# Kernel tuning notes

Measured on AMD Instinct MI355X. Metric: run time of the kernel, lower is better.

Reference implementation:

```python
import jax, jax.numpy as jnp
import numpy as np

B, N, D, H, DK, DV = 2, 2048, 1024, 16, 64, 64
NEG = -1000000000.0
EPS = 1e-6


def setup_inputs() -> dict:
    key = jax.random.key(0)
    ks = jax.random.split(key, 8)
    s = 0.02
    return {
        "q": jax.random.normal(ks[0], (B, N, D), jnp.float32),
        "k": jax.random.normal(ks[1], (B, N, D), jnp.float32),
        "v": jax.random.normal(ks[2], (B, N, D), jnp.float32),
        "attn_mask": jnp.ones((B, N, N), jnp.int32),
        "Wq": jax.random.normal(ks[3], (D, H * DK), jnp.float32) * s,
        "Wk": jax.random.normal(ks[4], (D, H * DK), jnp.float32) * s,
        "Wv": jax.random.normal(ks[5], (D, H * DV), jnp.float32) * s,
        "Wo": jax.random.normal(ks[6], (H * DV, D), jnp.float32) * s,
        "gamma": jnp.ones((D,), jnp.float32),
        "beta": jnp.zeros((D,), jnp.float32),
    }


def reference(q, k, v, attn_mask, Wq, Wk, Wv, Wo, gamma, beta):
    b, n, _ = q.shape
    residual = q
    # project and split heads: (b, h, n, dk)
    qh = (q @ Wq).reshape(b, n, H, DK).transpose(0, 2, 1, 3)
    kh = (k @ Wk).reshape(b, n, H, DK).transpose(0, 2, 1, 3)
    vh = (v @ Wv).reshape(b, n, H, DV).transpose(0, 2, 1, 3)
    temperature = DK ** 0.5
    scores = jnp.einsum('bhnd,bhmd->bhnm', qh / temperature, kh)
    # external mask (masked where mask == 0), broadcast over heads
    scores = jnp.where(attn_mask[:, None, :, :] == 0, NEG, scores)
    # built-in causal mask (strictly upper triangle)
    causal = jnp.triu(jnp.ones((n, n), dtype=bool), k=1)
    scores = jnp.where(causal, NEG, scores)
    attn = jax.nn.softmax(scores, axis=-1)
    out = jnp.einsum('bhnm,bhmd->bnhd', attn, vh).reshape(b, n, H * DV)
    out = out @ Wo + residual
    # LayerNorm(eps=1e-6)
    mean = out.mean(-1, keepdims=True)
    var = ((out - mean) ** 2).mean(-1, keepdims=True)
    out = (out - mean) / jnp.sqrt(var + EPS) * gamma + beta
    return out, attn
```

## Files before the change

kernel.cpp:

```cpp
#include <hip/hip_runtime.h>
#include <hip/hip_bf16.h>
#include <stdint.h>

#define B_ 2
#define N_ 2048
#define D_ 1024
#define H_ 16
#define MM 4096
#define NN 1024
#define KK 1024

typedef __bf16 bf16;
typedef __bf16 bf16x8 __attribute__((ext_vector_type(8)));
typedef float f32x4 __attribute__((ext_vector_type(4)));

struct __align__(8) bf4 { bf16 v[4]; };

#define LDS_STRIDE 144

#define GLDS(gp, lp)                                                     \
    __builtin_amdgcn_global_load_lds(                                    \
        (const __attribute__((address_space(1))) void*)(gp),             \
        (__attribute__((address_space(3))) void*)(lp), 16, 0, 0)

__global__ __launch_bounds__(256) void k_cvt3(const float* __restrict__ q,
                                              const float* __restrict__ k,
                                              const float* __restrict__ v,
                                              bf16* __restrict__ qb,
                                              bf16* __restrict__ kb,
                                              bf16* __restrict__ vb) {
    const int z = blockIdx.y;
    const float* s = z == 0 ? q : z == 1 ? k : v;
    bf16* d = z == 0 ? qb : z == 1 ? kb : vb;
    size_t i = ((size_t)blockIdx.x * 256 + threadIdx.x) * 8;
    f32x4 a = *(const f32x4*)(s + i);
    f32x4 b = *(const f32x4*)(s + i + 4);
    bf16x8 o;
#pragma unroll
    for (int j = 0; j < 4; ++j) { o[j] = (bf16)a[j]; o[4 + j] = (bf16)b[j]; }
    *(bf16x8*)(d + i) = o;
}

__global__ void k_wtt(const float* __restrict__ W, bf16* __restrict__ Wt) {
    __shared__ float t[32][33];
    int bx = blockIdx.x * 32, by = blockIdx.y * 32;
    int tx = threadIdx.x, ty = threadIdx.y;
#pragma unroll
    for (int j = 0; j < 32; j += 8)
        t[ty + j][tx] = W[(size_t)(by + ty + j) * 1024 + bx + tx];
    __syncthreads();
#pragma unroll
    for (int j = 0; j < 32; j += 8)
        Wt[(size_t)(bx + ty + j) * 1024 + by + tx] = (bf16)t[tx][ty + j];
}

__global__ __launch_bounds__(256) void k_bits(const int* __restrict__ mask,
                                              uint32_t* __restrict__ bits) {
    size_t flat = (size_t)blockIdx.x * 256 + threadIdx.x;
    int col = (int)(flat & (N_ - 1));
    int row = (int)((flat >> 11) & (N_ - 1));
    bool ok = (mask[flat] != 0) && (col <= row);
    unsigned long long bal = __ballot(ok);
    if ((threadIdx.x & 63) == 0)
        *(unsigned long long*)(bits + (flat >> 5)) = bal;
}

__device__ __forceinline__ void mm_core(const bf16* __restrict__ A,
                                        const bf16* __restrict__ Bt,
                                        int bm0, int bn0,
                                        bf16* As, bf16* Bs,
                                        f32x4 (&acc)[4][4]) {
    const int tid = threadIdx.x, w = tid >> 6, lane = tid & 63;
    const int g = lane >> 4, li = lane & 15;
    const int wr = w >> 1, wc = w & 1;
    const int row = tid >> 3, cc = tid & 7;

    f32x4 zz = {0.f, 0.f, 0.f, 0.f};
#pragma unroll
    for (int mf = 0; mf < 4; ++mf)
#pragma unroll
        for (int nf = 0; nf < 4; ++nf) acc[mf][nf] = zz;

    auto stage = [&](int k0) {
#pragma unroll
        for (int c = 0; c < 4; ++c) {
            int ch = c * 256 + tid;
            int r = ch >> 3, cl = ch & 7;
            GLDS(A + (size_t)(bm0 + r) * KK + k0 + cl * 8,
                 As + ((size_t)c * 256 + w * 64) * 8);
        }
#pragma unroll
        for (int c = 0; c < 4; ++c) {
            int ch = c * 256 + tid;
            int r = ch >> 3, cl = ch & 7;
            GLDS(Bt + (size_t)(bn0 + r) * KK + k0 + cl * 8,
                 Bs + ((size_t)c * 256 + w * 64) * 8);
        }
    };
    (void)row; (void)cc;

    stage(0);
    for (int s = 0; s < KK / 64; ++s) {
        __syncthreads();
#pragma unroll
        for (int kk = 0; kk < 2; ++kk) {
            bf16x8 af[4], bfr[4];
#pragma unroll
            for (int i = 0; i < 4; ++i) {
                af[i] = *(const bf16x8*)(As + (wr * 64 + i * 16 + li) * 64 + kk * 32 + g * 8);
                bfr[i] = *(const bf16x8*)(Bs + (wc * 64 + i * 16 + li) * 64 + kk * 32 + g * 8);
            }
#pragma unroll
            for (int mf = 0; mf < 4; ++mf)
#pragma unroll
                for (int nf = 0; nf < 4; ++nf)
                    acc[mf][nf] = __builtin_amdgcn_mfma_f32_16x16x32_bf16(
                        af[mf], bfr[nf], acc[mf][nf], 0, 0, 0);
        }
        __syncthreads();
        if (s + 1 < KK / 64) stage((s + 1) * 64);
    }
}

__global__ __launch_bounds__(256) void k_proj(const bf16* __restrict__ qb,
                                              const bf16* __restrict__ kb,
                                              const bf16* __restrict__ vb,
                                              const bf16* __restrict__ WqT,
                                              const bf16* __restrict__ WkT,
                                              const bf16* __restrict__ WvT,
                                              bf16* __restrict__ Qh,
                                              bf16* __restrict__ Kh,
                                              bf16* __restrict__ Vt) {
    __shared__ __align__(16) bf16 As[128 * 64];
    __shared__ __align__(16) bf16 Bs[128 * 64];
    const int z = blockIdx.y;
    const bf16* A = z == 0 ? qb : z == 1 ? kb : vb;
    const bf16* Bt = z == 0 ? WqT : z == 1 ? WkT : WvT;
    int bid = blockIdx.x;
    int swz = (bid & 7) * 32 + (bid >> 3);
    int bm0 = (swz >> 3) * 128, bn0 = (swz & 7) * 128;

    f32x4 acc[4][4];
    mm_core(A, Bt, bm0, bn0, As, Bs, acc);

    const int tid = threadIdx.x, w = tid >> 6, lane = tid & 63;
    const int g = lane >> 4, li = lane & 15;
    const int wr = w >> 1, wc = w & 1;
    const float scale = (z == 0) ? 0.125f : 1.0f;

    if (z < 2) {
        bf16* C = (z == 0) ? Qh : Kh;
#pragma unroll
        for (int mf = 0; mf < 4; ++mf)
#pragma unroll
            for (int nf = 0; nf < 4; ++nf) {
                int m0 = bm0 + wr * 64 + mf * 16 + g * 4;
                int n = bn0 + wc * 64 + nf * 16 + li;
#pragma unroll
                for (int r = 0; r < 4; ++r)
                    C[(size_t)(m0 + r) * NN + n] = (bf16)(acc[mf][nf][r] * scale);
            }
    } else {
#pragma unroll
        for (int mf = 0; mf < 4; ++mf)
#pragma unroll
            for (int nf = 0; nf < 4; ++nf) {
                int m0 = bm0 + wr * 64 + mf * 16 + g * 4;
                int n = bn0 + wc * 64 + nf * 16 + li;
                int bq = m0 >> 11, tok = m0 & (N_ - 1);
                int hh = n >> 6, dv = n & 63;
                bf4 val;
#pragma unroll
                for (int r = 0; r < 4; ++r) val.v[r] = (bf16)acc[mf][nf][r];
                *(bf4*)(Vt + ((size_t)((bq * H_ + hh) * 64 + dv)) * N_ + tok) = val;
            }
    }
}

__global__ __launch_bounds__(256) void k_out(const bf16* __restrict__ Ob,
                                             const bf16* __restrict__ WoT,
                                             float* __restrict__ outp,
                                             const float* __restrict__ resid) {
    __shared__ __align__(16) bf16 As[128 * 64];
    __shared__ __align__(16) bf16 Bs[128 * 64];
    int bid = blockIdx.x;
    int swz = (bid & 7) * 32 + (bid >> 3);
    int bm0 = (swz >> 3) * 128, bn0 = (swz & 7) * 128;

    f32x4 acc[4][4];
    mm_core(Ob, WoT, bm0, bn0, As, Bs, acc);

    const int tid = threadIdx.x, w = tid >> 6, lane = tid & 63;
    const int g = lane >> 4, li = lane & 15;
    const int wr = w >> 1, wc = w & 1;
#pragma unroll
    for (int mf = 0; mf < 4; ++mf)
#pragma unroll
        for (int nf = 0; nf < 4; ++nf) {
            int m0 = bm0 + wr * 64 + mf * 16 + g * 4;
            int n = bn0 + wc * 64 + nf * 16 + li;
#pragma unroll
            for (int r = 0; r < 4; ++r) {
                size_t ix = (size_t)(m0 + r) * NN + n;
                outp[ix] = acc[mf][nf][r] + resid[ix];
            }
        }
}

__global__ __launch_bounds__(256) void k_attn(const bf16* __restrict__ Qh,
                                              const bf16* __restrict__ Kh,
                                              const bf16* __restrict__ Vt,
                                              const uint32_t* __restrict__ bits,
                                              float* __restrict__ attnp,
                                              bf16* __restrict__ Ob) {
    __shared__ __align__(16) char Qs[64 * LDS_STRIDE];
    __shared__ __align__(16) char Ks[2][64 * LDS_STRIDE];
    __shared__ __align__(16) char Vs[2][64 * LDS_STRIDE];
    __shared__ __align__(16) char Ps[64 * LDS_STRIDE];
    const int tid = threadIdx.x, lane = tid & 63, w = tid >> 6;
    const int g = lane >> 4, li = lane & 15;
    const int p = blockIdx.x, h = blockIdx.y, b = blockIdx.z;
    const int srow = tid >> 3, sc = tid & 7;
    const int myrow = w * 16 + li;

    const size_t kbase = ((size_t)b * N_) * D_ + h * 64;
    const size_t vbase = ((size_t)(b * H_ + h) * 64) * N_;
    f32x4 zz = {0.f, 0.f, 0.f, 0.f};

    bf16x8 ka, kb2, va, vb2;
    auto loadK = [&](int jt) {
        const char* ks = (const char*)Kh +
            (kbase + (size_t)(jt * 64 + srow) * D_ + sc * 8) * 2;
        ka = *(const bf16x8*)ks;
        kb2 = *(const bf16x8*)(ks + (size_t)32 * D_ * 2);
    };
    auto loadV = [&](int jt) {
        const char* vs = (const char*)Vt +
            (vbase + (size_t)srow * N_ + jt * 64 + sc * 8) * 2;
        va = *(const bf16x8*)vs;
        vb2 = *(const bf16x8*)(vs + (size_t)32 * N_ * 2);
    };
    auto writeK = [&](int bi) {
        *(bf16x8*)(Ks[bi] + srow * LDS_STRIDE + sc * 16) = ka;
        *(bf16x8*)(Ks[bi] + (srow + 32) * LDS_STRIDE + sc * 16) = kb2;
    };
    auto writeV = [&](int bi) {
        *(bf16x8*)(Vs[bi] + srow * LDS_STRIDE + sc * 16) = va;
        *(bf16x8*)(Vs[bi] + (srow + 32) * LDS_STRIDE + sc * 16) = vb2;
    };

    for (int half = 0; half < 2; ++half) {
        const int qt = half ? (31 - p) : p;
        const int i0 = qt << 6;
        const size_t abase = (((size_t)b * H_ + h) * N_ + i0) * (size_t)N_;

        __syncthreads();
        {
            const char* qsrc = (const char*)Qh +
                (kbase + (size_t)(i0 + srow) * D_ + sc * 8) * 2;
            bf16x8 t0 = *(const bf16x8*)qsrc;
            bf16x8 t1 = *(const bf16x8*)(qsrc + (size_t)32 * D_ * 2);
            *(bf16x8*)(Qs + srow * LDS_STRIDE + sc * 16) = t0;
            *(bf16x8*)(Qs + (srow + 32) * LDS_STRIDE + sc * 16) = t1;
        }
        const uint32_t* mrow = bits + (((size_t)b * N_ + i0 + myrow) << 6);

        float m = -1e30f, l = 0.f;
        loadK(0);
        writeK(0);
        for (int jt = 0; jt <= qt; ++jt) {
            if (jt < qt) loadK(jt + 1);
            uint2 mw = *(const uint2*)(mrow + (jt << 1));
            __syncthreads();
            const char* Kb = Ks[jt & 1];

            f32x4 s[4];
#pragma unroll
            for (int mf = 0; mf < 4; ++mf) s[mf] = zz;
#pragma unroll
            for (int kk = 0; kk < 2; ++kk) {
                const int kb = kk * 64 + (g << 4);
                bf16x8 qf = *(const bf16x8*)(Qs + myrow * LDS_STRIDE + kb);
#pragma unroll
                for (int mf = 0; mf < 4; ++mf) {
                    bf16x8 kf = *(const bf16x8*)(Kb + (mf * 16 + li) * LDS_STRIDE + kb);
                    s[mf] = __builtin_amdgcn_mfma_f32_16x16x32_bf16(kf, qf, s[mf], 0, 0, 0);
                }
            }
            if (jt < qt) writeK((jt + 1) & 1);

            float tmax = m;
#pragma unroll
            for (int mf = 0; mf < 4; ++mf) {
                uint32_t wsel = (mf < 2) ? mw.x : mw.y;
#pragma unroll
                for (int r = 0; r < 4; ++r) {
                    int sh = (mf & 1) * 16 + g * 4 + r;
                    float xv = ((wsel >> sh) & 1) ? s[mf][r] : -1e9f;
                    s[mf][r] = xv;
                    tmax = fmaxf(tmax, xv);
                }
            }
            tmax = fmaxf(tmax, __shfl_xor(tmax, 16));
            tmax = fmaxf(tmax, __shfl_xor(tmax, 32));
            float ps = 0.f;
#pragma unroll
            for (int mf = 0; mf < 4; ++mf)
#pragma unroll
                for (int r = 0; r < 4; ++r) ps += __expf(s[mf][r] - tmax);
            ps += __shfl_xor(ps, 16);
            ps += __shfl_xor(ps, 32);
            l = l * __expf(m - tmax) + ps;
            m = tmax;
        }
        const float linv = 1.0f / l;

        f32x4 oacc[4];
#pragma unroll
        for (int nf = 0; nf < 4; ++nf) oacc[nf] = zz;

        __syncthreads();
        loadK(0);
        loadV(0);
        writeK(0);
        writeV(0);
        for (int jt = 0; jt <= qt; ++jt) {
            if (jt < qt) { loadK(jt + 1); loadV(jt + 1); }
            uint2 mw = *(const uint2*)(mrow + (jt << 1));
            __syncthreads();
            const char* Kb = Ks[jt & 1];
            const char* Vb = Vs[jt & 1];

            f32x4 s[4];
#pragma unroll
            for (int mf = 0; mf < 4; ++mf) s[mf] = zz;
#pragma unroll
            for (int kk = 0; kk < 2; ++kk) {
                const int kb = kk * 64 + (g << 4);
                bf16x8 qf = *(const bf16x8*)(Qs + myrow * LDS_STRIDE + kb);
#pragma unroll
                for (int mf = 0; mf < 4; ++mf) {
                    bf16x8 kf = *(const bf16x8*)(Kb + (mf * 16 + li) * LDS_STRIDE + kb);
                    s[mf] = __builtin_amdgcn_mfma_f32_16x16x32_bf16(kf, qf, s[mf], 0, 0, 0);
                }
            }
            if (jt < qt) { writeK((jt + 1) & 1); writeV((jt + 1) & 1); }

#pragma unroll
            for (int mf = 0; mf < 4; ++mf) {
                uint32_t wsel = (mf < 2) ? mw.x : mw.y;
#pragma unroll
                for (int r = 0; r < 4; ++r) {
                    int sh = (mf & 1) * 16 + g * 4 + r;
                    float xv = ((wsel >> sh) & 1) ? s[mf][r] : -1e9f;
                    s[mf][r] = __expf(xv - m) * linv;
                }
                __builtin_nontemporal_store(s[mf],
                    (f32x4*)(attnp + abase + (size_t)myrow * N_ + (jt << 6) + mf * 16 + g * 4));
                bf4 pk;
#pragma unroll
                for (int r = 0; r < 4; ++r) pk.v[r] = (bf16)s[mf][r];
                *(bf4*)(Ps + myrow * LDS_STRIDE + (mf * 16 + g * 4) * 2) = pk;
            }
#pragma unroll
            for (int kk = 0; kk < 2; ++kk) {
                const int kb = kk * 64 + (g << 4);
                bf16x8 pf = *(const bf16x8*)(Ps + myrow * LDS_STRIDE + kb);
#pragma unroll
                for (int nf = 0; nf < 4; ++nf) {
                    bf16x8 vf = *(const bf16x8*)(Vb + (nf * 16 + li) * LDS_STRIDE + kb);
                    oacc[nf] = __builtin_amdgcn_mfma_f32_16x16x32_bf16(pf, vf, oacc[nf], 0, 0, 0);
                }
            }
        }
#pragma unroll
        for (int nf = 0; nf < 4; ++nf)
#pragma unroll
            for (int r = 0; r < 4; ++r) {
                int gi = i0 + w * 16 + g * 4 + r;
                Ob[((size_t)(b * N_ + gi)) * D_ + h * 64 + nf * 16 + li] = (bf16)oacc[nf][r];
            }
        int zc0 = i0 + 64;
        if (zc0 < N_) {
            int r = tid >> 2, tc = tid & 3;
            f32x4 z = zz;
            for (int c = zc0 + tc * 4; c < N_; c += 16)
                __builtin_nontemporal_store(z, (f32x4*)(attnp + abase + (size_t)r * N_ + c));
        }
    }
}

__global__ __launch_bounds__(256) void k_ln(float* __restrict__ out,
                                            const float* __restrict__ gamma,
                                            const float* __restrict__ beta) {
    const int row = blockIdx.x, t = threadIdx.x, lane = t & 63, w = t >> 6;
    float* p = out + (size_t)row * D_;
    f32x4 x = *(const f32x4*)(p + t * 4);
    float s = x[0] + x[1] + x[2] + x[3];
    float s2 = x[0] * x[0] + x[1] * x[1] + x[2] * x[2] + x[3] * x[3];
#pragma unroll
    for (int o = 1; o < 64; o <<= 1) {
        s += __shfl_xor(s, o);
        s2 += __shfl_xor(s2, o);
    }
    __shared__ float r1[4], r2[4];
    if (lane == 0) { r1[w] = s; r2[w] = s2; }
    __syncthreads();
    s = r1[0] + r1[1] + r1[2] + r1[3];
    s2 = r2[0] + r2[1] + r2[2] + r2[3];
    float mean = s * (1.f / D_);
    float var = s2 * (1.f / D_) - mean * mean;
    float rstd = rsqrtf(var + 1e-6f);
    f32x4 gv = *(const f32x4*)(gamma + t * 4);
    f32x4 bv = *(const f32x4*)(beta + t * 4);
    f32x4 y;
#pragma unroll
    for (int c = 0; c < 4; ++c) y[c] = (x[c] - mean) * rstd * gv[c] + bv[c];
    *(f32x4*)(p + t * 4) = y;
}

extern "C" void kernel_launch(void* const* d_in, const int* in_sizes, int n_in,
                              void* d_out, int out_size, void* d_ws,
                              size_t ws_size, hipStream_t stream) {
    (void)in_sizes; (void)n_in; (void)out_size; (void)ws_size;
    const float* q = (const float*)d_in[0];
    const float* k = (const float*)d_in[1];
    const float* v = (const float*)d_in[2];
    const int* msk = (const int*)d_in[3];
    const float* Wq = (const float*)d_in[4];
    const float* Wk = (const float*)d_in[5];
    const float* Wv = (const float*)d_in[6];
    const float* Wo = (const float*)d_in[7];
    const float* gamma = (const float*)d_in[8];
    const float* beta = (const float*)d_in[9];

    float* outp = (float*)d_out;
    float* attnp = outp + (size_t)B_ * N_ * D_;

    const size_t U = (size_t)B_ * N_ * D_;
    const size_t W1 = (size_t)D_ * D_;
    bf16* ws = (bf16*)d_ws;
    bf16* qb = ws;   ws += U;
    bf16* kb = ws;   ws += U;
    bf16* vb = ws;   ws += U;
    bf16* WqT = ws;  ws += W1;
    bf16* WkT = ws;  ws += W1;
    bf16* WvT = ws;  ws += W1;
    bf16* WoT = ws;  ws += W1;
    bf16* Qh = ws;   ws += U;
    bf16* Kh = ws;   ws += U;
    bf16* Vt = ws;   ws += U;
    bf16* Ob = ws;   ws += U;
    uint32_t* bits = (uint32_t*)ws;

    k_cvt3<<<dim3(U / 8 / 256, 3), 256, 0, stream>>>(q, k, v, qb, kb, vb);
    dim3 tb(32, 8);
    k_wtt<<<dim3(32, 32), tb, 0, stream>>>(Wq, WqT);
    k_wtt<<<dim3(32, 32), tb, 0, stream>>>(Wk, WkT);
    k_wtt<<<dim3(32, 32), tb, 0, stream>>>(Wv, WvT);
    k_wtt<<<dim3(32, 32), tb, 0, stream>>>(Wo, WoT);
    k_bits<<<(size_t)B_ * N_ * N_ / 256, 256, 0, stream>>>(msk, bits);

    k_proj<<<dim3(256, 3), 256, 0, stream>>>(qb, kb, vb, WqT, WkT, WvT, Qh, Kh, Vt);

    k_attn<<<dim3(16, H_, B_), 256, 0, stream>>>(Qh, Kh, Vt, bits, attnp, Ob);

    k_out<<<256, 256, 0, stream>>>(Ob, WoT, outp, q);

    k_ln<<<B_ * N_, 256, 0, stream>>>(outp, gamma, beta);
}
```

Measured before the change: 300.2 us.

## Single-buffer K/V LDS, fold log2e into Q scale, merge weight transposes

The attention kernel drops the double-buffered K/V shared-memory tiles for a single buffer, with register prefetch of the next tile and an extra barrier per iteration. The softmax now uses exp2 with log2(e) folded into the Q projection scale, and m + log2(l) replaces the multiply by 1/l. The four weight-transpose launches are merged into one 3D-grid launch. The aim is less LDS (possibly higher occupancy), cheaper exponentials and fewer launches, at the cost of an extra sync per tile and less load/compute overlap.

```diff
diff --git a/kernel.cpp b/kernel.cpp
--- a/kernel.cpp
+++ b/kernel.cpp
@@ -17,6 +17,7 @@
 struct __align__(8) bf4 { bf16 v[4]; };
 
 #define LDS_STRIDE 144
+#define LOG2E 1.44269504088896340736f
 
 #define GLDS(gp, lp)                                                     \
     __builtin_amdgcn_global_load_lds(                                    \
@@ -41,7 +42,13 @@
     *(bf16x8*)(d + i) = o;
 }
 
-__global__ void k_wtt(const float* __restrict__ W, bf16* __restrict__ Wt) {
+__global__ void k_wtt4(const float* __restrict__ Wq, const float* __restrict__ Wk,
+                       const float* __restrict__ Wv, const float* __restrict__ Wo,
+                       bf16* __restrict__ WqT, bf16* __restrict__ WkT,
+                       bf16* __restrict__ WvT, bf16* __restrict__ WoT) {
+    const int z = blockIdx.z;
+    const float* W = z == 0 ? Wq : z == 1 ? Wk : z == 2 ? Wv : Wo;
+    bf16* Wt = z == 0 ? WqT : z == 1 ? WkT : z == 2 ? WvT : WoT;
     __shared__ float t[32][33];
     int bx = blockIdx.x * 32, by = blockIdx.y * 32;
     int tx = threadIdx.x, ty = threadIdx.y;
@@ -73,7 +80,6 @@
     const int tid = threadIdx.x, w = tid >> 6, lane = tid & 63;
     const int g = lane >> 4, li = lane & 15;
     const int wr = w >> 1, wc = w & 1;
-    const int row = tid >> 3, cc = tid & 7;
 
     f32x4 zz = {0.f, 0.f, 0.f, 0.f};
 #pragma unroll
@@ -97,7 +103,6 @@
                  Bs + ((size_t)c * 256 + w * 64) * 8);
         }
     };
-    (void)row; (void)cc;
 
     stage(0);
     for (int s = 0; s < KK / 64; ++s) {
@@ -146,7 +151,7 @@
     const int tid = threadIdx.x, w = tid >> 6, lane = tid & 63;
     const int g = lane >> 4, li = lane & 15;
     const int wr = w >> 1, wc = w & 1;
-    const float scale = (z == 0) ? 0.125f : 1.0f;
+    const float scale = (z == 0) ? 0.125f * LOG2E : 1.0f;
 
     if (z < 2) {
         bf16* C = (z == 0) ? Qh : Kh;
@@ -214,8 +219,8 @@
                                               float* __restrict__ attnp,
                                               bf16* __restrict__ Ob) {
     __shared__ __align__(16) char Qs[64 * LDS_STRIDE];
-    __shared__ __align__(16) char Ks[2][64 * LDS_STRIDE];
-    __shared__ __align__(16) char Vs[2][64 * LDS_STRIDE];
+    __shared__ __align__(16) char Ks[64 * LDS_STRIDE];
+    __shared__ __align__(16) char Vs[64 * LDS_STRIDE];
     __shared__ __align__(16) char Ps[64 * LDS_STRIDE];
     const int tid = threadIdx.x, lane = tid & 63, w = tid >> 6;
     const int g = lane >> 4, li = lane & 15;
@@ -226,28 +231,6 @@
     const size_t kbase = ((size_t)b * N_) * D_ + h * 64;
     const size_t vbase = ((size_t)(b * H_ + h) * 64) * N_;
     f32x4 zz = {0.f, 0.f, 0.f, 0.f};
-
-    bf16x8 ka, kb2, va, vb2;
-    auto loadK = [&](int jt) {
-        const char* ks = (const char*)Kh +
-            (kbase + (size_t)(jt * 64 + srow) * D_ + sc * 8) * 2;
-        ka = *(const bf16x8*)ks;
-        kb2 = *(const bf16x8*)(ks + (size_t)32 * D_ * 2);
-    };
-    auto loadV = [&](int jt) {
-        const char* vs = (const char*)Vt +
-            (vbase + (size_t)srow * N_ + jt * 64 + sc * 8) * 2;
-        va = *(const bf16x8*)vs;
-        vb2 = *(const bf16x8*)(vs + (size_t)32 * N_ * 2);
-    };
-    auto writeK = [&](int bi) {
-        *(bf16x8*)(Ks[bi] + srow * LDS_STRIDE + sc * 16) = ka;
-        *(bf16x8*)(Ks[bi] + (srow + 32) * LDS_STRIDE + sc * 16) = kb2;
-    };
-    auto writeV = [&](int bi) {
-        *(bf16x8*)(Vs[bi] + srow * LDS_STRIDE + sc * 16) = va;
-        *(bf16x8*)(Vs[bi] + (srow + 32) * LDS_STRIDE + sc * 16) = vb2;
-    };
 
     for (int half = 0; half < 2; ++half) {
         const int qt = half ? (31 - p) : p;
@@ -266,13 +249,25 @@
         const uint32_t* mrow = bits + (((size_t)b * N_ + i0 + myrow) << 6);
 
         float m = -1e30f, l = 0.f;
-        loadK(0);
-        writeK(0);
+        bf16x8 ka, kb2, va, vb2;
+        {
+            const char* ks = (const char*)Kh + (kbase + (size_t)srow * D_ + sc * 8) * 2;
+            ka = *(const bf16x8*)ks;
+            kb2 = *(const bf16x8*)(ks + (size_t)32 * D_ * 2);
+        }
         for (int jt = 0; jt <= qt; ++jt) {
-            if (jt < qt) loadK(jt + 1);
+            __syncthreads();
+            *(bf16x8*)(Ks + srow * LDS_STRIDE + sc * 16) = ka;
+            *(bf16x8*)(Ks + (srow + 32) * LDS_STRIDE + sc * 16) = kb2;
+            {
+                int jn = (jt < qt) ? jt + 1 : qt;
+                const char* ks = (const char*)Kh +
+                    (kbase + (size_t)(jn * 64 + srow) * D_ + sc * 8) * 2;
+                ka = *(const bf16x8*)ks;
+                kb2 = *(const bf16x8*)(ks + (size_t)32 * D_ * 2);
+            }
             uint2 mw = *(const uint2*)(mrow + (jt << 1));
             __syncthreads();
-            const char* Kb = Ks[jt & 1];
 
             f32x4 s[4];
 #pragma unroll
@@ -283,12 +278,10 @@
                 bf16x8 qf = *(const bf16x8*)(Qs + myrow * LDS_STRIDE + kb);
 #pragma unroll
                 for (int mf = 0; mf < 4; ++mf) {
-                    bf16x8 kf = *(const bf16x8*)(Kb + (mf * 16 + li) * LDS_STRIDE + kb);
+                    bf16x8 kf = *(const bf16x8*)(Ks + (mf * 16 + li) * LDS_STRIDE + kb);
                     s[mf] = __builtin_amdgcn_mfma_f32_16x16x32_bf16(kf, qf, s[mf], 0, 0, 0);
                 }
             }
-            if (jt < qt) writeK((jt + 1) & 1);
-
             float tmax = m;
 #pragma unroll
             for (int mf = 0; mf < 4; ++mf) {
@@ -307,29 +300,45 @@
 #pragma unroll
             for (int mf = 0; mf < 4; ++mf)
 #pragma unroll
-                for (int r = 0; r < 4; ++r) ps += __expf(s[mf][r] - tmax);
+                for (int r = 0; r < 4; ++r) ps += exp2f(s[mf][r] - tmax);
             ps += __shfl_xor(ps, 16);
             ps += __shfl_xor(ps, 32);
-            l = l * __expf(m - tmax) + ps;
+            l = l * exp2f(m - tmax) + ps;
             m = tmax;
         }
-        const float linv = 1.0f / l;
+        const float ml = m + __log2f(l);
 
         f32x4 oacc[4];
 #pragma unroll
         for (int nf = 0; nf < 4; ++nf) oacc[nf] = zz;
 
-        __syncthreads();
-        loadK(0);
-        loadV(0);
-        writeK(0);
-        writeV(0);
+        {
+            const char* ks = (const char*)Kh + (kbase + (size_t)srow * D_ + sc * 8) * 2;
+            ka = *(const bf16x8*)ks;
+            kb2 = *(const bf16x8*)(ks + (size_t)32 * D_ * 2);
+            const char* vs = (const char*)Vt + (vbase + (size_t)srow * N_ + sc * 8) * 2;
+            va = *(const bf16x8*)vs;
+            vb2 = *(const bf16x8*)(vs + (size_t)32 * N_ * 2);
+        }
         for (int jt = 0; jt <= qt; ++jt) {
-            if (jt < qt) { loadK(jt + 1); loadV(jt + 1); }
+            __syncthreads();
+            *(bf16x8*)(Ks + srow * LDS_STRIDE + sc * 16) = ka;
+            *(bf16x8*)(Ks + (srow + 32) * LDS_STRIDE + sc * 16) = kb2;
+            *(bf16x8*)(Vs + srow * LDS_STRIDE + sc * 16) = va;
+            *(bf16x8*)(Vs + (srow + 32) * LDS_STRIDE + sc * 16) = vb2;
+            {
+                int jn = (jt < qt) ? jt + 1 : qt;
+                const char* ks = (const char*)Kh +
+                    (kbase + (size_t)(jn * 64 + srow) * D_ + sc * 8) * 2;
+                ka = *(const bf16x8*)ks;
+                kb2 = *(const bf16x8*)(ks + (size_t)32 * D_ * 2);
+                const char* vs = (const char*)Vt +
+                    (vbase + (size_t)srow * N_ + jn * 64 + sc * 8) * 2;
+                va = *(const bf16x8*)vs;
+                vb2 = *(const bf16x8*)(vs + (size_t)32 * N_ * 2);
+            }
             uint2 mw = *(const uint2*)(mrow + (jt << 1));
             __syncthreads();
-            const char* Kb = Ks[jt & 1];
-            const char* Vb = Vs[jt & 1];
 
             f32x4 s[4];
 #pragma unroll
@@ -340,11 +349,10 @@
                 bf16x8 qf = *(const bf16x8*)(Qs + myrow * LDS_STRIDE + kb);
 #pragma unroll
                 for (int mf = 0; mf < 4; ++mf) {
-                    bf16x8 kf = *(const bf16x8*)(Kb + (mf * 16 + li) * LDS_STRIDE + kb);
+                    bf16x8 kf = *(const bf16x8*)(Ks + (mf * 16 + li) * LDS_STRIDE + kb);
                     s[mf] = __builtin_amdgcn_mfma_f32_16x16x32_bf16(kf, qf, s[mf], 0, 0, 0);
                 }
             }
-            if (jt < qt) { writeK((jt + 1) & 1); writeV((jt + 1) & 1); }
 
 #pragma unroll
             for (int mf = 0; mf < 4; ++mf) {
@@ -353,7 +361,7 @@
                 for (int r = 0; r < 4; ++r) {
                     int sh = (mf & 1) * 16 + g * 4 + r;
                     float xv = ((wsel >> sh) & 1) ? s[mf][r] : -1e9f;
-                    s[mf][r] = __expf(xv - m) * linv;
+                    s[mf][r] = exp2f(xv - ml);
                 }
                 __builtin_nontemporal_store(s[mf],
                     (f32x4*)(attnp + abase + (size_t)myrow * N_ + (jt << 6) + mf * 16 + g * 4));
@@ -368,7 +376,7 @@
                 bf16x8 pf = *(const bf16x8*)(Ps + myrow * LDS_STRIDE + kb);
 #pragma unroll
                 for (int nf = 0; nf < 4; ++nf) {
-                    bf16x8 vf = *(const bf16x8*)(Vb + (nf * 16 + li) * LDS_STRIDE + kb);
+                    bf16x8 vf = *(const bf16x8*)(Vs + (nf * 16 + li) * LDS_STRIDE + kb);
                     oacc[nf] = __builtin_amdgcn_mfma_f32_16x16x32_bf16(pf, vf, oacc[nf], 0, 0, 0);
                 }
             }
@@ -454,11 +462,7 @@
     uint32_t* bits = (uint32_t*)ws;
 
     k_cvt3<<<dim3(U / 8 / 256, 3), 256, 0, stream>>>(q, k, v, qb, kb, vb);
-    dim3 tb(32, 8);
-    k_wtt<<<dim3(32, 32), tb, 0, stream>>>(Wq, WqT);
-    k_wtt<<<dim3(32, 32), tb, 0, stream>>>(Wk, WkT);
-    k_wtt<<<dim3(32, 32), tb, 0, stream>>>(Wv, WvT);
-    k_wtt<<<dim3(32, 32), tb, 0, stream>>>(Wo, WoT);
+    k_wtt4<<<dim3(32, 32, 4), dim3(32, 8), 0, stream>>>(Wq, Wk, Wv, Wo, WqT, WkT, WvT, WoT);
     k_bits<<<(size_t)B_ * N_ * N_ / 256, 256, 0, stream>>>(msk, bits);
 
     k_proj<<<dim3(256, 3), 256, 0, stream>>>(qb, kb, vb, WqT, WkT, WvT, Qh, Kh, Vt);
```

Result: slower. 306.8 us (+2.2%).
